# Kernel optimization log

Measured on AMD Instinct MI355X. Metric: run time of the kernel, lower is better.

## Reference

```python
import jax, jax.numpy as jnp
import numpy as np

MARGIN = 0.1

def setup_inputs() -> dict:
    key = jax.random.key(0)
    k1, k2 = jax.random.split(key)
    embeddings = jax.random.normal(k1, (8192, 128), dtype=jnp.float32)
    labels = jax.random.randint(k2, (8192,), 0, 64, dtype=jnp.int64)
    return {"embeddings": embeddings, "labels": labels}

def reference(embeddings, labels):
    # sim[i,j] = <e_i, e_j>
    sim = embeddings @ embeddings.T  # [n, n]
    eq = labels[:, None] == labels[None, :]  # pos mask (includes diagonal)
    # per entry: exp(margin - sim) for positives, exp(sim - margin) for negatives
    terms = jnp.where(eq, jnp.exp(MARGIN - sim), jnp.exp(sim - MARGIN))
    # loss_i = log(sum_j terms[i,j]); loss = mean_i loss_i
    return jnp.mean(jnp.log(jnp.sum(terms, axis=1)))
```

## Files before the change

### kernel.cpp

```cpp
#include <hip/hip_runtime.h>
#include <hip/hip_bf16.h>

#define N 8192
#define D 128
#define LOG2E  1.44269504088896f
#define LN2    0.69314718055995f

#define COLSB   272
#define NSTEPS  4

typedef __attribute__((ext_vector_type(8))) short bf16x8;
typedef __attribute__((ext_vector_type(4))) float f32x4;

#if __has_builtin(__builtin_amdgcn_exp2f)
#define EXP2(x) __builtin_amdgcn_exp2f(x)
#else
#define EXP2(x) exp2f(x)
#endif
#if __has_builtin(__builtin_amdgcn_logf)
#define LOG2(x) __builtin_amdgcn_logf(x)
#else
#define LOG2(x) log2f(x)
#endif

static __device__ __forceinline__ unsigned short f2bf(float f) {
    union { float f; unsigned int u; } x;
    x.f = f;
    unsigned int r = ((x.u >> 16) & 1u) + 0x7FFFu;
    return (unsigned short)((x.u + r) >> 16);
}

__global__ void prep_kernel(const float* __restrict__ E,
                            unsigned short* __restrict__ Eb,
                            float* __restrict__ rowsum,
                            float* __restrict__ out) {
    int idx = blockIdx.x * 256 + threadIdx.x;
    float4 v = ((const float4*)E)[idx];
    ushort4 o;
    o.x = f2bf(v.x); o.y = f2bf(v.y); o.z = f2bf(v.z); o.w = f2bf(v.w);
    ((ushort4*)Eb)[idx] = o;
    if (idx < N) rowsum[idx] = 0.0f;
    if (idx == 0) out[0] = 0.0f;
}

__global__ __launch_bounds__(128) void fused_kernel(
        const unsigned short* __restrict__ Eb,
        const int* __restrict__ labels,
        float* __restrict__ rowsum) {
    __shared__ __align__(16) char ldsbuf[2][32 * COLSB];

    const int tid  = threadIdx.x;
    const int wid  = tid >> 6;
    const int lane = tid & 63;
    const int q = lane >> 4;
    const int l = lane & 15;

    const int b = blockIdx.x;
    int r = (int)(64.5f - sqrtf(64.5f * 64.5f - 2.0f * (float)b));
    while ((r + 1) * 64 - ((r + 1) * r) / 2 <= b) ++r;
    while (r * 64 - (r * (r - 1)) / 2 > b) --r;
    const int c = r + (b - (r * 64 - (r * (r - 1)) / 2));
    const bool diag = (r == c);
    const int m0 = r * 128 + wid * 64;
    const int n_begin = c * 128;

    bf16x8 a[4][4];
#pragma unroll
    for (int g = 0; g < 4; ++g) {
        const bf16x8* p = (const bf16x8*)(Eb + (size_t)(m0 + g * 16 + l) * D + q * 8);
#pragma unroll
        for (int kk = 0; kk < 4; ++kk) a[g][kk] = p[kk * 4];
    }

    int lrow[16];
#pragma unroll
    for (int g = 0; g < 4; ++g)
#pragma unroll
        for (int rr = 0; rr < 4; ++rr)
            lrow[g * 4 + rr] = labels[m0 + g * 16 + q * 4 + rr];

    float sum[16];
#pragma unroll
    for (int i = 0; i < 16; ++i) sum[i] = 0.0f;

    const char* gB = (const char*)Eb + (size_t)n_begin * 256;
    const int gofs = tid * 64;
    const int lofs = (tid >> 2) * COLSB + (tid & 3) * 64;

    float4 v0, v1, v2, v3;
    {
        const float4* p = (const float4*)(gB + gofs);
        v0 = p[0]; v1 = p[1]; v2 = p[2]; v3 = p[3];
        float4* dst = (float4*)(&ldsbuf[0][lofs]);
        dst[0] = v0; dst[1] = v1; dst[2] = v2; dst[3] = v3;
        const float4* p1 = (const float4*)(gB + 32 * 256 + gofs);
        v0 = p1[0]; v1 = p1[1]; v2 = p1[2]; v3 = p1[3];
    }
    __syncthreads();

#pragma clang loop unroll(disable)
    for (int t = 0; t < NSTEPS; ++t) {
        if (t + 1 < NSTEPS) {
            float4* dst = (float4*)(&ldsbuf[(t + 1) & 1][lofs]);
            dst[0] = v0; dst[1] = v1; dst[2] = v2; dst[3] = v3;
        }
        if (t + 2 < NSTEPS) {
            const float4* p = (const float4*)(gB + (size_t)(t + 2) * 32 * 256 + gofs);
            v0 = p[0]; v1 = p[1]; v2 = p[2]; v3 = p[3];
        }

#pragma unroll
        for (int s = 0; s < 2; ++s) {
            const int col = n_begin + t * 32 + s * 16 + l;
            const int lc = labels[col];
            const char* lb = &ldsbuf[t & 1][(s * 16 + l) * COLSB + q * 16];
            bf16x8 b0 = *(const bf16x8*)(lb);
            bf16x8 b1 = *(const bf16x8*)(lb + 64);
            bf16x8 b2 = *(const bf16x8*)(lb + 128);
            bf16x8 b3 = *(const bf16x8*)(lb + 192);

            f32x4 acc[4];
#pragma unroll
            for (int g = 0; g < 4; ++g) {
                acc[g] = (f32x4){0.f, 0.f, 0.f, 0.f};
                acc[g] = __builtin_amdgcn_mfma_f32_16x16x32_bf16(a[g][0], b0, acc[g], 0, 0, 0);
                acc[g] = __builtin_amdgcn_mfma_f32_16x16x32_bf16(a[g][1], b1, acc[g], 0, 0, 0);
                acc[g] = __builtin_amdgcn_mfma_f32_16x16x32_bf16(a[g][2], b2, acc[g], 0, 0, 0);
                acc[g] = __builtin_amdgcn_mfma_f32_16x16x32_bf16(a[g][3], b3, acc[g], 0, 0, 0);
            }

            float cp = 0.0f;
#pragma unroll
            for (int g = 0; g < 4; ++g) {
#pragma unroll
                for (int rr = 0; rr < 4; ++rr) {
                    float sv = acc[g][rr];
                    bool eq = (lrow[g * 4 + rr] == lc);
                    float cc = eq ? -LOG2E : LOG2E;
                    float term = EXP2(cc * (sv - 0.1f));
                    sum[g * 4 + rr] += term;
                    cp += term;
                }
            }
            if (!diag) {
                cp += __shfl_xor(cp, 16);
                cp += __shfl_xor(cp, 32);
                if (q == 0) atomicAdd(&rowsum[col], cp);
            }
        }
        __syncthreads();
    }

#pragma unroll
    for (int i = 0; i < 16; ++i) {
        float v = sum[i];
        v += __shfl_xor(v, 1);
        v += __shfl_xor(v, 2);
        v += __shfl_xor(v, 4);
        v += __shfl_xor(v, 8);
        sum[i] = v;
    }
    if (l == 0) {
#pragma unroll
        for (int g = 0; g < 4; ++g)
#pragma unroll
            for (int rr = 0; rr < 4; ++rr)
                atomicAdd(&rowsum[m0 + g * 16 + q * 4 + rr], sum[g * 4 + rr]);
    }
}

__global__ void finalize_kernel(const float* __restrict__ rowsum, float* __restrict__ out) {
    __shared__ float red[4];
    int i = blockIdx.x * 256 + threadIdx.x;
    float v = LOG2(rowsum[i]) * LN2;
#pragma unroll
    for (int off = 1; off <= 32; off <<= 1) v += __shfl_xor(v, off);
    if ((threadIdx.x & 63) == 0) red[threadIdx.x >> 6] = v;
    __syncthreads();
    if (threadIdx.x == 0)
        atomicAdd(out, (red[0] + red[1] + red[2] + red[3]) * (1.0f / (float)N));
}

extern "C" void kernel_launch(void* const* d_in, const int* in_sizes, int n_in,
                              void* d_out, int out_size, void* d_ws, size_t ws_size,
                              hipStream_t stream) {
    const float* E = (const float*)d_in[0];
    const int* labels = (const int*)d_in[1];
    float* out = (float*)d_out;

    unsigned short* Eb = (unsigned short*)d_ws;
    float* rowsum = (float*)((char*)d_ws + (size_t)N * D * sizeof(unsigned short));

    prep_kernel<<<1024, 256, 0, stream>>>(E, Eb, rowsum, out);
    fused_kernel<<<2080, 128, 0, stream>>>(Eb, labels, rowsum);
    finalize_kernel<<<32, 256, 0, stream>>>(rowsum, out);
}
```

Baseline: 99.15 us.

## Use 256-thread blocks, load whole B tile once, accumulate column sums in LDS

Each block now has 4 waves, each owning 32 rows, instead of 2 waves owning 64 rows. The whole 128-column B tile and both label vectors are staged into LDS in one shot, which removes the double-buffered pipeline and the per-step barriers. Per-column partial sums are accumulated with LDS atomics and flushed to global memory once per block, replacing many global atomics. In exchange there is more LDS per block, no overlap between the load and compute phases, and fewer MFMAs per B fragment read from LDS.

```diff
diff --git a/kernel.cpp b/kernel.cpp
--- a/kernel.cpp
+++ b/kernel.cpp
@@ -5,9 +5,7 @@
 #define D 128
 #define LOG2E  1.44269504088896f
 #define LN2    0.69314718055995f
-
-#define COLSB   272
-#define NSTEPS  4
+#define COLSB  272
 
 typedef __attribute__((ext_vector_type(8))) short bf16x8;
 typedef __attribute__((ext_vector_type(4))) float f32x4;
@@ -43,11 +41,14 @@
     if (idx == 0) out[0] = 0.0f;
 }
 
-__global__ __launch_bounds__(128) void fused_kernel(
+__global__ __launch_bounds__(256) void fused_kernel(
         const unsigned short* __restrict__ Eb,
         const int* __restrict__ labels,
         float* __restrict__ rowsum) {
-    __shared__ __align__(16) char ldsbuf[2][32 * COLSB];
+    __shared__ __align__(16) char bB[128 * COLSB];
+    __shared__ int   labC[128];
+    __shared__ int   labR[128];
+    __shared__ float colacc[128];
 
     const int tid  = threadIdx.x;
     const int wid  = tid >> 6;
@@ -61,98 +62,87 @@
     while (r * 64 - (r * (r - 1)) / 2 > b) --r;
     const int c = r + (b - (r * 64 - (r * (r - 1)) / 2));
     const bool diag = (r == c);
-    const int m0 = r * 128 + wid * 64;
+    const int tile_m0 = r * 128;
     const int n_begin = c * 128;
+    const int mrow0 = tile_m0 + wid * 32;
 
-    bf16x8 a[4][4];
+    bf16x8 a[2][4];
 #pragma unroll
-    for (int g = 0; g < 4; ++g) {
-        const bf16x8* p = (const bf16x8*)(Eb + (size_t)(m0 + g * 16 + l) * D + q * 8);
+    for (int g = 0; g < 2; ++g) {
+        const bf16x8* p = (const bf16x8*)(Eb + (size_t)(mrow0 + g * 16 + l) * D + q * 8);
 #pragma unroll
         for (int kk = 0; kk < 4; ++kk) a[g][kk] = p[kk * 4];
     }
+    const char* gB = (const char*)Eb + (size_t)n_begin * 256;
+    const int col  = tid >> 1;
+    const int half = tid & 1;
+    const float4* src = (const float4*)(gB + col * 256 + half * 128);
+    float4 st[8];
+#pragma unroll
+    for (int i = 0; i < 8; ++i) st[i] = src[i];
+    int labv = (tid < 128) ? labels[n_begin + tid]
+                           : labels[tile_m0 + (tid - 128)];
 
-    int lrow[16];
+    float4* dst = (float4*)(bB + col * COLSB + half * 128);
 #pragma unroll
-    for (int g = 0; g < 4; ++g)
+    for (int i = 0; i < 8; ++i) dst[i] = st[i];
+    if (tid < 128) { labC[tid] = labv; colacc[tid] = 0.0f; }
+    else           { labR[tid - 128] = labv; }
+    __syncthreads();
+
+    int lrow[8];
+#pragma unroll
+    for (int g = 0; g < 2; ++g)
 #pragma unroll
         for (int rr = 0; rr < 4; ++rr)
-            lrow[g * 4 + rr] = labels[m0 + g * 16 + q * 4 + rr];
+            lrow[g * 4 + rr] = labR[wid * 32 + g * 16 + q * 4 + rr];
 
-    float sum[16];
+    float sum[8];
 #pragma unroll
-    for (int i = 0; i < 16; ++i) sum[i] = 0.0f;
-
-    const char* gB = (const char*)Eb + (size_t)n_begin * 256;
-    const int gofs = tid * 64;
-    const int lofs = (tid >> 2) * COLSB + (tid & 3) * 64;
-
-    float4 v0, v1, v2, v3;
-    {
-        const float4* p = (const float4*)(gB + gofs);
-        v0 = p[0]; v1 = p[1]; v2 = p[2]; v3 = p[3];
-        float4* dst = (float4*)(&ldsbuf[0][lofs]);
-        dst[0] = v0; dst[1] = v1; dst[2] = v2; dst[3] = v3;
-        const float4* p1 = (const float4*)(gB + 32 * 256 + gofs);
-        v0 = p1[0]; v1 = p1[1]; v2 = p1[2]; v3 = p1[3];
-    }
-    __syncthreads();
+    for (int i = 0; i < 8; ++i) sum[i] = 0.0f;
 
 #pragma clang loop unroll(disable)
-    for (int t = 0; t < NSTEPS; ++t) {
-        if (t + 1 < NSTEPS) {
-            float4* dst = (float4*)(&ldsbuf[(t + 1) & 1][lofs]);
-            dst[0] = v0; dst[1] = v1; dst[2] = v2; dst[3] = v3;
-        }
-        if (t + 2 < NSTEPS) {
-            const float4* p = (const float4*)(gB + (size_t)(t + 2) * 32 * 256 + gofs);
-            v0 = p[0]; v1 = p[1]; v2 = p[2]; v3 = p[3];
-        }
+    for (int s = 0; s < 8; ++s) {
+        const int lc = labC[s * 16 + l];
+        const char* lb = bB + (s * 16 + l) * COLSB + q * 16;
+        bf16x8 b0 = *(const bf16x8*)(lb);
+        bf16x8 b1 = *(const bf16x8*)(lb + 64);
+        bf16x8 b2 = *(const bf16x8*)(lb + 128);
+        bf16x8 b3 = *(const bf16x8*)(lb + 192);
 
+        f32x4 acc0 = (f32x4){0.f, 0.f, 0.f, 0.f};
+        f32x4 acc1 = (f32x4){0.f, 0.f, 0.f, 0.f};
+        acc0 = __builtin_amdgcn_mfma_f32_16x16x32_bf16(a[0][0], b0, acc0, 0, 0, 0);
+        acc0 = __builtin_amdgcn_mfma_f32_16x16x32_bf16(a[0][1], b1, acc0, 0, 0, 0);
+        acc0 = __builtin_amdgcn_mfma_f32_16x16x32_bf16(a[0][2], b2, acc0, 0, 0, 0);
+        acc0 = __builtin_amdgcn_mfma_f32_16x16x32_bf16(a[0][3], b3, acc0, 0, 0, 0);
+        acc1 = __builtin_amdgcn_mfma_f32_16x16x32_bf16(a[1][0], b0, acc1, 0, 0, 0);
+        acc1 = __builtin_amdgcn_mfma_f32_16x16x32_bf16(a[1][1], b1, acc1, 0, 0, 0);
+        acc1 = __builtin_amdgcn_mfma_f32_16x16x32_bf16(a[1][2], b2, acc1, 0, 0, 0);
+        acc1 = __builtin_amdgcn_mfma_f32_16x16x32_bf16(a[1][3], b3, acc1, 0, 0, 0);
+
+        float cp = 0.0f;
 #pragma unroll
-        for (int s = 0; s < 2; ++s) {
-            const int col = n_begin + t * 32 + s * 16 + l;
-            const int lc = labels[col];
-            const char* lb = &ldsbuf[t & 1][(s * 16 + l) * COLSB + q * 16];
-            bf16x8 b0 = *(const bf16x8*)(lb);
-            bf16x8 b1 = *(const bf16x8*)(lb + 64);
-            bf16x8 b2 = *(const bf16x8*)(lb + 128);
-            bf16x8 b3 = *(const bf16x8*)(lb + 192);
-
-            f32x4 acc[4];
+        for (int g = 0; g < 2; ++g) {
 #pragma unroll
-            for (int g = 0; g < 4; ++g) {
-                acc[g] = (f32x4){0.f, 0.f, 0.f, 0.f};
-                acc[g] = __builtin_amdgcn_mfma_f32_16x16x32_bf16(a[g][0], b0, acc[g], 0, 0, 0);
-                acc[g] = __builtin_amdgcn_mfma_f32_16x16x32_bf16(a[g][1], b1, acc[g], 0, 0, 0);
-                acc[g] = __builtin_amdgcn_mfma_f32_16x16x32_bf16(a[g][2], b2, acc[g], 0, 0, 0);
-                acc[g] = __builtin_amdgcn_mfma_f32_16x16x32_bf16(a[g][3], b3, acc[g], 0, 0, 0);
-            }
-
-            float cp = 0.0f;
-#pragma unroll
-            for (int g = 0; g < 4; ++g) {
-#pragma unroll
-                for (int rr = 0; rr < 4; ++rr) {
-                    float sv = acc[g][rr];
-                    bool eq = (lrow[g * 4 + rr] == lc);
-                    float cc = eq ? -LOG2E : LOG2E;
-                    float term = EXP2(cc * (sv - 0.1f));
-                    sum[g * 4 + rr] += term;
-                    cp += term;
-                }
-            }
-            if (!diag) {
-                cp += __shfl_xor(cp, 16);
-                cp += __shfl_xor(cp, 32);
-                if (q == 0) atomicAdd(&rowsum[col], cp);
+            for (int rr = 0; rr < 4; ++rr) {
+                float sv = (g == 0) ? acc0[rr] : acc1[rr];
+                bool eq = (lrow[g * 4 + rr] == lc);
+                float cc = eq ? -LOG2E : LOG2E;
+                float term = EXP2(cc * (sv - 0.1f));
+                sum[g * 4 + rr] += term;
+                cp += term;
             }
         }
-        __syncthreads();
+        if (!diag) {
+            cp += __shfl_xor(cp, 16);
+            cp += __shfl_xor(cp, 32);
+            if (q == 0) atomicAdd(&colacc[s * 16 + l], cp);
+        }
     }
 
 #pragma unroll
-    for (int i = 0; i < 16; ++i) {
+    for (int i = 0; i < 8; ++i) {
         float v = sum[i];
         v += __shfl_xor(v, 1);
         v += __shfl_xor(v, 2);
@@ -162,11 +152,14 @@
     }
     if (l == 0) {
 #pragma unroll
-        for (int g = 0; g < 4; ++g)
+        for (int g = 0; g < 2; ++g)
 #pragma unroll
             for (int rr = 0; rr < 4; ++rr)
-                atomicAdd(&rowsum[m0 + g * 16 + q * 4 + rr], sum[g * 4 + rr]);
+                atomicAdd(&rowsum[mrow0 + g * 16 + q * 4 + rr], sum[g * 4 + rr]);
     }
+
+    __syncthreads();
+    if (!diag && tid < 128) atomicAdd(&rowsum[n_begin + tid], colacc[tid]);
 }
 
 __global__ void finalize_kernel(const float* __restrict__ rowsum, float* __restrict__ out) {
@@ -192,6 +185,6 @@
     float* rowsum = (float*)((char*)d_ws + (size_t)N * D * sizeof(unsigned short));
 
     prep_kernel<<<1024, 256, 0, stream>>>(E, Eb, rowsum, out);
-    fused_kernel<<<2080, 128, 0, stream>>>(Eb, labels, rowsum);
+    fused_kernel<<<2080, 256, 0, stream>>>(Eb, labels, rowsum);
     finalize_kernel<<<32, 256, 0, stream>>>(rowsum, out);
 }
```

Result: faster. 90.88 us (-8.3%).
